# Optimization experiments

Measured on AMD Instinct MI355X. Metric: run time of the kernel, lower is better.

Reference implementation:

```python
import jax, jax.numpy as jnp
import numpy as np

NUM_NODES = 20000
NUM_RELATIONS = 32
HIDDEN = 128
EMB = 16
NUM_EDGES = 600000


def setup_inputs() -> dict:
    key = jax.random.key(0)
    ks = jax.random.split(key, 8)
    edge_index = jax.random.randint(ks[0], (2, NUM_EDGES), 0, NUM_NODES, dtype=jnp.int64)
    edge_type = jax.random.randint(ks[1], (NUM_EDGES,), 0, NUM_RELATIONS, dtype=jnp.int64)
    node_emb = jax.random.normal(ks[2], (NUM_NODES, EMB), dtype=jnp.float32)
    W1 = jax.random.normal(ks[3], (NUM_RELATIONS, EMB, HIDDEN), dtype=jnp.float32) * (1.0 / np.sqrt(EMB))
    root1 = jax.random.normal(ks[4], (EMB, HIDDEN), dtype=jnp.float32) * (1.0 / np.sqrt(EMB))
    b1 = jnp.zeros((HIDDEN,), dtype=jnp.float32)
    W2 = jax.random.normal(ks[5], (NUM_RELATIONS, HIDDEN, HIDDEN), dtype=jnp.float32) * (1.0 / np.sqrt(HIDDEN))
    root2 = jax.random.normal(ks[6], (HIDDEN, HIDDEN), dtype=jnp.float32) * (1.0 / np.sqrt(HIDDEN))
    b2 = jnp.zeros((HIDDEN,), dtype=jnp.float32)
    return {"edge_index": edge_index, "edge_type": edge_type, "node_emb": node_emb,
            "W1": W1, "root1": root1, "b1": b1, "W2": W2, "root2": root2, "b2": b2}


def rgcn_layer(x, edge_index, edge_type, W, root, bias):
    # PyG RGCNConv: per-relation transform, per-(dst, relation) MEAN aggregation,
    # summed over relations, plus root transform and bias.
    src, dst = edge_index[0], edge_index[1]
    # mean normalization per (dst, relation) segment
    seg = dst * NUM_RELATIONS + edge_type                      # [E]
    counts = jax.ops.segment_sum(jnp.ones(seg.shape, jnp.float32), seg,
                                 num_segments=NUM_NODES * NUM_RELATIONS)
    inv = jnp.where(counts > 0, 1.0 / counts, 0.0)
    # transform every node by every relation weight: [N, R, H]
    xr = jnp.einsum('nf,rfh->nrh', x, W)
    msg = xr[src, edge_type] * inv[seg][:, None]               # [E, H]
    agg = jax.ops.segment_sum(msg, dst, num_segments=NUM_NODES)  # [N, H]
    return agg + x @ root + bias


def reference(edge_index, edge_type, node_emb, W1, root1, b1, W2, root2, b2):
    h = rgcn_layer(node_emb, edge_index, edge_type, W1, root1, b1)
    h = jax.nn.relu(h)
    h = rgcn_layer(h, edge_index, edge_type, W2, root2, b2)
    return h
```

## Files before the change

### kernel.cpp

```cpp
#include <hip/hip_runtime.h>
#include <hip/hip_bf16.h>

#define N_NODES 20000
#define N_REL 32
#define HID 128
#define EMB 16
#define N_EDGES 600000
#define NB (N_NODES * N_REL)

typedef __attribute__((ext_vector_type(8))) short  bf8v;
typedef __attribute__((ext_vector_type(8))) unsigned short us8v;
typedef __attribute__((ext_vector_type(4))) unsigned short us4v;
typedef __attribute__((ext_vector_type(4))) float  f4v;

__device__ __forceinline__ unsigned short f2b(float f) {
    __hip_bfloat16 h = __float2bfloat16(f);
    return __builtin_bit_cast(unsigned short, h);
}
__device__ __forceinline__ float b2f(unsigned short u) {
    unsigned int x = ((unsigned int)u) << 16;
    return __builtin_bit_cast(float, x);
}

__device__ __forceinline__ void lds_barrier() {
    asm volatile("s_waitcnt lgkmcnt(0)\n\ts_barrier" ::: "memory");
}

#define R_W2 (N_REL * HID * HID)
#define R_XB (N_NODES * 32)
#define R_W1 (N_REL * HID * 32)
#define R_R1 (HID * 32)
#define R_R2 (HID * HID)
#define R_HIST N_EDGES
#define PRE_TOT (R_W2 + R_XB + R_W1 + R_R1 + R_R2 + R_HIST)

__global__ __launch_bounds__(256) void pre1_k(
    const int* __restrict__ dst, const int* __restrict__ et,
    const float* __restrict__ x, const float* __restrict__ W1,
    const float* __restrict__ root1, const float* __restrict__ W2,
    const float* __restrict__ root2,
    int* __restrict__ hist,
    unsigned short* __restrict__ xb, unsigned short* __restrict__ w1t,
    unsigned short* __restrict__ r1t, unsigned short* __restrict__ w2t,
    unsigned short* __restrict__ r2t) {
    int i = blockIdx.x * 256 + threadIdx.x;
    if (i < R_W2) {
        int r = i >> 14, k = (i >> 7) & 127, n = i & 127;
        int ct8 = n >> 4, m16 = n & 15, ks = k >> 5, q = (k >> 3) & 3, j = k & 7;
        w2t[(size_t)r * 16384 + (ct8 * 4 + ks) * 512 + m16 * 32 + q * 8 + j] = f2b(W2[i]);
        return;
    }
    i -= R_W2;
    if (i < R_XB) {
        int n = i >> 5, k = i & 31;
        xb[i] = (k < EMB) ? f2b(x[n * EMB + k]) : (unsigned short)0;
        return;
    }
    i -= R_XB;
    if (i < R_W1) {
        int r = i >> 12, rem = i & 4095;
        int ct8 = rem >> 9, m16 = (rem >> 5) & 15, q = (rem >> 3) & 3, j = rem & 7;
        int n = ct8 * 16 + m16, k = q * 8 + j;
        w1t[i] = (k < EMB) ? f2b(W1[(r << 11) + (k << 7) + n]) : (unsigned short)0;
        return;
    }
    i -= R_W1;
    if (i < R_R1) {
        int ct8 = i >> 9, m16 = (i >> 5) & 15, q = (i >> 3) & 3, j = i & 7;
        int n = ct8 * 16 + m16, k = q * 8 + j;
        r1t[i] = (k < EMB) ? f2b(root1[(k << 7) + n]) : (unsigned short)0;
        return;
    }
    i -= R_R1;
    if (i < R_R2) {
        int ct8 = i >> 11, ks = (i >> 9) & 3, m16 = (i >> 5) & 15, q = (i >> 3) & 3, j = i & 7;
        int n = ct8 * 16 + m16, k = ks * 32 + q * 8 + j;
        r2t[i] = f2b(root2[(k << 7) + n]);
        return;
    }
    i -= R_R2;
    if (i < R_HIST) atomicAdd(&hist[dst[i] * N_REL + et[i]], 1);
}

__global__ void scan1_k(const int* __restrict__ hist, int* __restrict__ binoff,
                        int* __restrict__ bsum, float* __restrict__ inv) {
    __shared__ int sh[256];
    const int t = threadIdx.x;
    const int base = blockIdx.x * 1024 + t * 4;
    int4 h4 = *(const int4*)(hist + base);
    float4 iv4;
    iv4.x = h4.x > 0 ? 1.0f / h4.x : 0.0f;
    iv4.y = h4.y > 0 ? 1.0f / h4.y : 0.0f;
    iv4.z = h4.z > 0 ? 1.0f / h4.z : 0.0f;
    iv4.w = h4.w > 0 ? 1.0f / h4.w : 0.0f;
    *(float4*)(inv + base) = iv4;
    int ts = h4.x + h4.y + h4.z + h4.w;
    sh[t] = ts;
    __syncthreads();
    for (int o = 1; o < 256; o <<= 1) {
        int v = (t >= o) ? sh[t - o] : 0;
        __syncthreads();
        sh[t] += v;
        __syncthreads();
    }
    int exc = sh[t] - ts;
    binoff[base + 0] = exc;
    binoff[base + 1] = exc + h4.x;
    binoff[base + 2] = exc + h4.x + h4.y;
    binoff[base + 3] = exc + h4.x + h4.y + h4.z;
    if (t == 255) bsum[blockIdx.x] = sh[255];
}

__global__ void scan2_k(const int* __restrict__ bsum, int* __restrict__ bbase) {
    __shared__ int sh[1024];
    const int t = threadIdx.x;
    int v = (t < 625) ? bsum[t] : 0;
    sh[t] = v;
    __syncthreads();
    for (int o = 1; o < 1024; o <<= 1) {
        int u = (t >= o) ? sh[t - o] : 0;
        __syncthreads();
        sh[t] += u;
        __syncthreads();
    }
    if (t < 625) bbase[t] = sh[t] - v;
}

__global__ void scan3_k(int* __restrict__ binoff, const int* __restrict__ bbase,
                        int* __restrict__ cursors) {
    int i = blockIdx.x * 256 + threadIdx.x;
    if (i < NB) {
        int v = binoff[i] + bbase[i >> 10];
        binoff[i] = v;
        cursors[i] = v;
    }
    if (i == 0) binoff[NB] = N_EDGES;
}

__global__ void scatter_k(const int* __restrict__ src, const int* __restrict__ dst,
                          const int* __restrict__ et, int* __restrict__ cursors,
                          int* __restrict__ ssrc) {
    int e = blockIdx.x * 256 + threadIdx.x;
    if (e < 4) ssrc[N_EDGES + e] = 0;
    if (e < N_EDGES) {
        int b = dst[e] * N_REL + et[e];
        int p = atomicAdd(&cursors[b], 1);
        ssrc[p] = src[e];
    }
}

template<int KT, int LSS, int CW, int RG>
__global__ __launch_bounds__(256) void gemm_f(
    const int* __restrict__ binoff, const float* __restrict__ inv,
    const int* __restrict__ ssrc,
    const unsigned short* __restrict__ G,
    const unsigned short* __restrict__ Bw,
    const unsigned short* __restrict__ Br,
    float* __restrict__ part) {

    constexpr int ROW = KT * 32;
    constexpr int NCH = ROW / CW;
    constexpr int CP8 = CW / 8;
    static_assert(NCH * CW == ROW, "chunk covering must be exact");
    static_assert(32 * NCH <= 256, "one gather item per thread");

    __shared__ __align__(16) unsigned short As[2][32 * LSS];
    __shared__ int   smO[32 * (RG + 1)];
    __shared__ float smI[32 * RG];

    const int t = threadIdx.x;
    const int w = t >> 6, lane = t & 63;
    const int q = lane >> 4, m16 = lane & 15;
    const int d0 = blockIdx.x * 32;
    const int r0 = blockIdx.y * RG;
    const bool isLast = (blockIdx.y == gridDim.y - 1);
    const int colb = w * 32;
    const int cb16 = colb >> 4;
    const int fo = m16 * 32 + q * 8;
    const bool gat = t < 32 * NCH;
    const int grow = t / NCH, gcc = t % NCH;
    const int mb  = grow * (RG + 1);
    const int mbI = grow * RG;
    int uo[CP8];
#pragma unroll
    for (int j = 0; j < CP8; ++j) uo[j] = (gcc + j * NCH) * 8;

    for (int i = t; i < 32 * (RG + 1); i += 256) {
        int row = i / (RG + 1), rr = i % (RG + 1);
        smO[i] = binoff[(d0 + row) * N_REL + r0 + rr];
    }
    for (int i = t; i < 32 * RG; i += 256) {
        int row = i / RG, rr = i % RG;
        smI[i] = inv[(d0 + row) * N_REL + r0 + rr];
    }
    lds_barrier();

    f4v acc[2][2];
#pragma unroll
    for (int rt = 0; rt < 2; ++rt)
#pragma unroll
        for (int ct = 0; ct < 2; ++ct) acc[rt][ct] = f4v{0.f, 0.f, 0.f, 0.f};

    us8v gE[4][CP8];
#pragma unroll
    for (int e = 0; e < 4; ++e)
#pragma unroll
        for (int j = 0; j < CP8; ++j) gE[e][j] = us8v{};
    int sx[4] = {0, 0, 0, 0};

    if (gat) {
        const int so = smO[mb], cnt = smO[mb + 1] - so;
        int s0 = ssrc[so], s1 = ssrc[so + 1], s2 = ssrc[so + 2], s3 = ssrc[so + 3];
        if (cnt >= 1) {
            const unsigned short* gp = G + (size_t)s0 * ROW;
#pragma unroll
            for (int j = 0; j < CP8; ++j) gE[0][j] = *(const us8v*)(gp + uo[j]);
        }
        if (cnt >= 2) {
            const unsigned short* gp = G + (size_t)s1 * ROW;
#pragma unroll
            for (int j = 0; j < CP8; ++j) gE[1][j] = *(const us8v*)(gp + uo[j]);
        }
        if (cnt >= 3) {
            const unsigned short* gp = G + (size_t)s2 * ROW;
#pragma unroll
            for (int j = 0; j < CP8; ++j) gE[2][j] = *(const us8v*)(gp + uo[j]);
        }
        if (cnt >= 4) {
            const unsigned short* gp = G + (size_t)s3 * ROW;
#pragma unroll
            for (int j = 0; j < CP8; ++j) gE[3][j] = *(const us8v*)(gp + uo[j]);
        }
        if (RG > 1) {
            const int so1 = smO[mb + 1];
            sx[0] = ssrc[so1]; sx[1] = ssrc[so1 + 1];
            sx[2] = ssrc[so1 + 2]; sx[3] = ssrc[so1 + 3];
        }
    }

    bf8v bfr[2][KT];
#pragma unroll
    for (int ct = 0; ct < 2; ++ct) {
#pragma unroll
        for (int ks = 0; ks < KT; ++ks)
            bfr[ct][ks] = *(const bf8v*)(Bw + (size_t)r0 * (HID * ROW)
                              + ((cb16 + ct) * KT + ks) * 512 + fo);
    }

    for (int it = 0; it < RG; ++it) {
        unsigned short* Ab = As[it & 1];
        if (gat) {
            const int so = smO[mb + it], eo = smO[mb + it + 1];
            const int cnt = eo - so;
            const float m2 = cnt >= 2 ? 1.f : 0.f;
            const float m3 = cnt >= 3 ? 1.f : 0.f;
            const float m4 = cnt >= 4 ? 1.f : 0.f;
            float a[CW];
#pragma unroll
            for (int j = 0; j < CP8; ++j)
#pragma unroll
                for (int k = 0; k < 8; ++k)
                    a[j * 8 + k] = b2f(gE[0][j][k]) + m2 * b2f(gE[1][j][k])
                                 + m3 * b2f(gE[2][j][k]) + m4 * b2f(gE[3][j][k]);
            for (int p = so + 4; p < eo; ++p) {
                const unsigned short* gp = G + (size_t)ssrc[p] * ROW;
#pragma unroll
                for (int j = 0; j < CP8; ++j) {
                    us8v g = *(const us8v*)(gp + uo[j]);
#pragma unroll
                    for (int k = 0; k < 8; ++k) a[j * 8 + k] += b2f(g[k]);
                }
            }
            const float iv = smI[mbI + it];
            unsigned short* wp = &Ab[grow * LSS];
#pragma unroll
            for (int j = 0; j < CP8; ++j) {
                us8v sv;
#pragma unroll
                for (int k = 0; k < 8; ++k) sv[k] = f2b(a[j * 8 + k] * iv);
                *(us8v*)(wp + uo[j]) = sv;
            }

            if (it + 1 < RG) {
                const int c1 = smO[mb + it + 2] - smO[mb + it + 1];
                if (c1 >= 1) {
                    const unsigned short* gp = G + (size_t)sx[0] * ROW;
#pragma unroll
                    for (int j = 0; j < CP8; ++j) gE[0][j] = *(const us8v*)(gp + uo[j]);
                }
                if (c1 >= 2) {
                    const unsigned short* gp = G + (size_t)sx[1] * ROW;
#pragma unroll
                    for (int j = 0; j < CP8; ++j) gE[1][j] = *(const us8v*)(gp + uo[j]);
                }
                if (c1 >= 3) {
                    const unsigned short* gp = G + (size_t)sx[2] * ROW;
#pragma unroll
                    for (int j = 0; j < CP8; ++j) gE[2][j] = *(const us8v*)(gp + uo[j]);
                }
                if (c1 >= 4) {
                    const unsigned short* gp = G + (size_t)sx[3] * ROW;
#pragma unroll
                    for (int j = 0; j < CP8; ++j) gE[3][j] = *(const us8v*)(gp + uo[j]);
                }
                if (it + 2 < RG) {
                    const int so2 = smO[mb + it + 2];
                    sx[0] = ssrc[so2]; sx[1] = ssrc[so2 + 1];
                    sx[2] = ssrc[so2 + 2]; sx[3] = ssrc[so2 + 3];
                }
            }
        }
        lds_barrier();

#pragma unroll
        for (int rt = 0; rt < 2; ++rt) {
            const unsigned short* ar = &Ab[(m16 + 16 * rt) * LSS];
#pragma unroll
            for (int ks = 0; ks < KT; ++ks) {
                bf8v af = *(const bf8v*)(ar + ks * 32 + q * 8);
                acc[rt][0] = __builtin_amdgcn_mfma_f32_16x16x32_bf16(af, bfr[0][ks], acc[rt][0], 0, 0, 0);
                acc[rt][1] = __builtin_amdgcn_mfma_f32_16x16x32_bf16(af, bfr[1][ks], acc[rt][1], 0, 0, 0);
            }
        }

        const unsigned short* Bp = (it + 1 < RG) ? (Bw + (size_t)(r0 + it + 1) * (HID * ROW))
                                                 : (isLast ? Br : nullptr);
        if (Bp) {
#pragma unroll
            for (int ct = 0; ct < 2; ++ct) {
#pragma unroll
                for (int ks = 0; ks < KT; ++ks)
                    bfr[ct][ks] = *(const bf8v*)(Bp + ((cb16 + ct) * KT + ks) * 512 + fo);
            }
        }
    }

    if (isLast) {
#pragma unroll
        for (int rt = 0; rt < 2; ++rt) {
#pragma unroll
            for (int ks = 0; ks < KT; ++ks) {
                bf8v af = *(const bf8v*)(G + (size_t)(d0 + m16 + 16 * rt) * ROW + ks * 32 + q * 8);
                acc[rt][0] = __builtin_amdgcn_mfma_f32_16x16x32_bf16(af, bfr[0][ks], acc[rt][0], 0, 0, 0);
                acc[rt][1] = __builtin_amdgcn_mfma_f32_16x16x32_bf16(af, bfr[1][ks], acc[rt][1], 0, 0, 0);
            }
        }
    }

    float* pb = part + (size_t)blockIdx.y * N_NODES * HID;
#pragma unroll
    for (int ct = 0; ct < 2; ++ct) {
        const int col = colb + 16 * ct + m16;
#pragma unroll
        for (int rt = 0; rt < 2; ++rt) {
#pragma unroll
            for (int g = 0; g < 4; ++g) {
                const int rr = 16 * rt + q * 4 + g;
                __builtin_nontemporal_store(acc[rt][ct][g],
                    &pb[(size_t)(d0 + rr) * HID + col]);
            }
        }
    }
}

__global__ __launch_bounds__(256) void reduce1_k(
    const float* __restrict__ part, const float* __restrict__ b1,
    unsigned short* __restrict__ h1b) {
    int i = blockIdx.x * 256 + threadIdx.x;
    if (i >= N_NODES * HID / 4) return;
    const size_t S = (size_t)N_NODES * HID;
    float4 bb = *(const float4*)(b1 + ((i * 4) & 127));
    float r0 = bb.x, r1 = bb.y, r2 = bb.z, r3 = bb.w;
#pragma unroll
    for (int p = 0; p < 2; ++p) {
        const float* pp = part + p * S + (size_t)i * 4;
        r0 += __builtin_nontemporal_load(pp + 0);
        r1 += __builtin_nontemporal_load(pp + 1);
        r2 += __builtin_nontemporal_load(pp + 2);
        r3 += __builtin_nontemporal_load(pp + 3);
    }
    us4v v;
    v[0] = f2b(fmaxf(r0, 0.0f));
    v[1] = f2b(fmaxf(r1, 0.0f));
    v[2] = f2b(fmaxf(r2, 0.0f));
    v[3] = f2b(fmaxf(r3, 0.0f));
    *(us4v*)(h1b + (size_t)i * 4) = v;
}

__global__ __launch_bounds__(256) void reduce2_k(
    const float* __restrict__ part, const float* __restrict__ b2,
    float* __restrict__ out) {
    int i = blockIdx.x * 256 + threadIdx.x;
    if (i >= N_NODES * HID / 4) return;
    const size_t S = (size_t)N_NODES * HID;
    float4 bb = *(const float4*)(b2 + ((i * 4) & 127));
    float r0 = bb.x, r1 = bb.y, r2 = bb.z, r3 = bb.w;
#pragma unroll
    for (int p = 0; p < 4; ++p) {
        const float* pp = part + p * S + (size_t)i * 4;
        r0 += __builtin_nontemporal_load(pp + 0);
        r1 += __builtin_nontemporal_load(pp + 1);
        r2 += __builtin_nontemporal_load(pp + 2);
        r3 += __builtin_nontemporal_load(pp + 3);
    }
    float4 r; r.x = r0; r.y = r1; r.z = r2; r.w = r3;
    ((float4*)out)[i] = r;
}

extern "C" void kernel_launch(void* const* d_in, const int* in_sizes, int n_in,
                              void* d_out, int out_size, void* d_ws, size_t ws_size,
                              hipStream_t stream) {
    const int*   ei    = (const int*)d_in[0];
    const int*   et    = (const int*)d_in[1];
    const float* x     = (const float*)d_in[2];
    const float* W1    = (const float*)d_in[3];
    const float* root1 = (const float*)d_in[4];
    const float* b1    = (const float*)d_in[5];
    const float* W2    = (const float*)d_in[6];
    const float* root2 = (const float*)d_in[7];
    const float* b2    = (const float*)d_in[8];
    float* out = (float*)d_out;

    char* ws = (char*)d_ws;
    size_t off = 0;
    auto alloc = [&](size_t bytes) { void* p = ws + off; off = (off + bytes + 63) & ~(size_t)63; return p; };
    int*   hist    = (int*)  alloc((size_t)NB * 4);
    int*   binoff  = (int*)  alloc((size_t)(NB + 1) * 4);
    int*   cursors = (int*)  alloc((size_t)NB * 4);
    float* inv     = (float*)alloc((size_t)NB * 4);
    int*   bsum    = (int*)  alloc(625 * 4);
    int*   bbase   = (int*)  alloc(625 * 4);
    int*   ssrc    = (int*)  alloc((size_t)(N_EDGES + 4) * 4);
    unsigned short* xb  = (unsigned short*)alloc((size_t)N_NODES * 32 * 2);
    unsigned short* h1b = (unsigned short*)alloc((size_t)N_NODES * HID * 2);
    unsigned short* w1t = (unsigned short*)alloc((size_t)N_REL * HID * 32 * 2);
    unsigned short* r1t = (unsigned short*)alloc((size_t)HID * 32 * 2);
    unsigned short* w2t = (unsigned short*)alloc((size_t)N_REL * HID * HID * 2);
    unsigned short* r2t = (unsigned short*)alloc((size_t)HID * HID * 2);
    float* part = (float*)alloc((size_t)4 * N_NODES * HID * 4);

    const int* src = ei;
    const int* dst = ei + N_EDGES;

    hipMemsetAsync(hist, 0, (size_t)NB * 4, stream);
    pre1_k<<<(PRE_TOT + 255) / 256, 256, 0, stream>>>(
        dst, et, x, W1, root1, W2, root2, hist, xb, w1t, r1t, w2t, r2t);
    scan1_k<<<NB / 1024, 256, 0, stream>>>(hist, binoff, bsum, inv);
    scan2_k<<<1, 1024, 0, stream>>>(bsum, bbase);
    scan3_k<<<(NB + 255) / 256, 256, 0, stream>>>(binoff, bbase, cursors);
    scatter_k<<<(N_EDGES + 255) / 256, 256, 0, stream>>>(src, dst, et, cursors, ssrc);

    gemm_f<1, 40, 8, 16><<<dim3(625, 2), 256, 0, stream>>>(
        binoff, inv, ssrc, xb, w1t, r1t, part);
    reduce1_k<<<(N_NODES * HID / 4 + 255) / 256, 256, 0, stream>>>(part, b1, h1b);

    gemm_f<4, 136, 16, 8><<<dim3(625, 4), 256, 0, stream>>>(
        binoff, inv, ssrc, h1b, w2t, r2t, part);
    reduce2_k<<<(N_NODES * HID / 4 + 255) / 256, 256, 0, stream>>>(part, b2, out);
}
```

Before: 247.0 us.

## Pack multiple relations per K-tile in layer 1 and fuse its reduction

Layer 1 used to zero-pad the 16-wide embedding to 32 so that each MFMA K-step carried one relation. It now packs two relations, each 16 wide, into every K=32 step and gathers 8 relation segments per iteration in unpadded bf16. Layer 1 runs as a single grid column, so bias, ReLU and the bf16 cast are applied in the epilogue, which removes the partial buffer and the reduce1 kernel. The weight layouts are rebuilt to a K-block-major order to match, and root1 is zero-padded for the partial K tile. The aim is to halve the wasted MFMA and gather work in layer 1 and cut one launch plus its memory traffic, at the cost of less grid parallelism for layer 1.

```diff
diff --git a/kernel.cpp b/kernel.cpp
--- a/kernel.cpp
+++ b/kernel.cpp
@@ -27,8 +27,8 @@
 }
 
 #define R_W2 (N_REL * HID * HID)
-#define R_XB (N_NODES * 32)
-#define R_W1 (N_REL * HID * 32)
+#define R_XB (N_NODES * EMB)
+#define R_W1 (N_REL * EMB * HID)
 #define R_R1 (HID * 32)
 #define R_R2 (HID * HID)
 #define R_HIST N_EDGES
@@ -46,36 +46,34 @@
     int i = blockIdx.x * 256 + threadIdx.x;
     if (i < R_W2) {
         int r = i >> 14, k = (i >> 7) & 127, n = i & 127;
-        int ct8 = n >> 4, m16 = n & 15, ks = k >> 5, q = (k >> 3) & 3, j = k & 7;
-        w2t[(size_t)r * 16384 + (ct8 * 4 + ks) * 512 + m16 * 32 + q * 8 + j] = f2b(W2[i]);
+        int kb = r * 4 + (k >> 5), q = (k >> 3) & 3, j = k & 7;
+        int ct8 = n >> 4, m16 = n & 15;
+        w2t[(size_t)kb * 4096 + ct8 * 512 + m16 * 32 + q * 8 + j] = f2b(W2[i]);
         return;
     }
     i -= R_W2;
-    if (i < R_XB) {
-        int n = i >> 5, k = i & 31;
-        xb[i] = (k < EMB) ? f2b(x[n * EMB + k]) : (unsigned short)0;
-        return;
-    }
+    if (i < R_XB) { xb[i] = f2b(x[i]); return; }
     i -= R_XB;
     if (i < R_W1) {
-        int r = i >> 12, rem = i & 4095;
-        int ct8 = rem >> 9, m16 = (rem >> 5) & 15, q = (rem >> 3) & 3, j = rem & 7;
-        int n = ct8 * 16 + m16, k = q * 8 + j;
-        w1t[i] = (k < EMB) ? f2b(W1[(r << 11) + (k << 7) + n]) : (unsigned short)0;
+        int rel = i >> 11, kk = (i >> 7) & 15, n = i & 127;
+        int kb = rel >> 1, k = ((rel & 1) << 4) + kk;
+        int q = k >> 3, j = k & 7, ct8 = n >> 4, m16 = n & 15;
+        w1t[kb * 4096 + ct8 * 512 + m16 * 32 + q * 8 + j] = f2b(W1[i]);
         return;
     }
     i -= R_W1;
     if (i < R_R1) {
-        int ct8 = i >> 9, m16 = (i >> 5) & 15, q = (i >> 3) & 3, j = i & 7;
-        int n = ct8 * 16 + m16, k = q * 8 + j;
-        r1t[i] = (k < EMB) ? f2b(root1[(k << 7) + n]) : (unsigned short)0;
+        int k = i >> 7, n = i & 127;
+        int q = k >> 3, j = k & 7, ct8 = n >> 4, m16 = n & 15;
+        r1t[ct8 * 512 + m16 * 32 + q * 8 + j] =
+            (k < EMB) ? f2b(root1[k * 128 + n]) : (unsigned short)0;
         return;
     }
     i -= R_R1;
     if (i < R_R2) {
-        int ct8 = i >> 11, ks = (i >> 9) & 3, m16 = (i >> 5) & 15, q = (i >> 3) & 3, j = i & 7;
-        int n = ct8 * 16 + m16, k = ks * 32 + q * 8 + j;
-        r2t[i] = f2b(root2[(k << 7) + n]);
+        int k = i >> 7, n = i & 127;
+        int ks = k >> 5, q = (k >> 3) & 3, j = k & 7, ct8 = n >> 4, m16 = n & 15;
+        r2t[(ks * 8 + ct8) * 512 + m16 * 32 + q * 8 + j] = f2b(root2[i]);
         return;
     }
     i -= R_R2;
@@ -149,20 +147,26 @@
     }
 }
 
-template<int KT, int LSS, int CW, int RG>
+template<int ROWG, int NRC, int NIT, int KR, bool FUSE>
 __global__ __launch_bounds__(256) void gemm_f(
     const int* __restrict__ binoff, const float* __restrict__ inv,
     const int* __restrict__ ssrc,
     const unsigned short* __restrict__ G,
     const unsigned short* __restrict__ Bw,
     const unsigned short* __restrict__ Br,
-    float* __restrict__ part) {
-
-    constexpr int ROW = KT * 32;
-    constexpr int NCH = ROW / CW;
+    float* __restrict__ part, unsigned short* __restrict__ fout,
+    const float* __restrict__ bias) {
+
+    constexpr int RG  = NRC * NIT;
+    constexpr int KT  = (NRC * ROWG) / 32;
+    constexpr int NCH = 256 / (32 * NRC);
+    constexpr int CW  = ROWG / NCH;
     constexpr int CP8 = CW / 8;
-    static_assert(NCH * CW == ROW, "chunk covering must be exact");
-    static_assert(32 * NCH <= 256, "one gather item per thread");
+    constexpr int LSS = NRC * ROWG + 8;
+    static_assert(NCH * CW == ROWG, "chunk covering must be exact");
+    static_assert(CP8 * 8 == CW, "16B unit covering");
+    static_assert(KT * 32 == NRC * ROWG, "K must be a multiple of 32");
+    static_assert(32 * NRC * NCH == 256, "all threads gather");
 
     __shared__ __align__(16) unsigned short As[2][32 * LSS];
     __shared__ int   smO[32 * (RG + 1)];
@@ -177,13 +181,15 @@
     const int colb = w * 32;
     const int cb16 = colb >> 4;
     const int fo = m16 * 32 + q * 8;
-    const bool gat = t < 32 * NCH;
-    const int grow = t / NCH, gcc = t % NCH;
-    const int mb  = grow * (RG + 1);
-    const int mbI = grow * RG;
+    const int brow = t / (NRC * NCH);
+    const int rsub = (t / NCH) % NRC;
+    const int gcc  = t % NCH;
+    const int mb  = brow * (RG + 1) + rsub;
+    const int mbI = brow * RG + rsub;
     int uo[CP8];
 #pragma unroll
     for (int j = 0; j < CP8; ++j) uo[j] = (gcc + j * NCH) * 8;
+    const int lbase = brow * LSS + rsub * ROWG;
 
     for (int i = t; i < 32 * (RG + 1); i += 256) {
         int row = i / (RG + 1), rr = i % (RG + 1);
@@ -208,49 +214,51 @@
         for (int j = 0; j < CP8; ++j) gE[e][j] = us8v{};
     int sx[4] = {0, 0, 0, 0};
 
-    if (gat) {
+    {
         const int so = smO[mb], cnt = smO[mb + 1] - so;
         int s0 = ssrc[so], s1 = ssrc[so + 1], s2 = ssrc[so + 2], s3 = ssrc[so + 3];
         if (cnt >= 1) {
-            const unsigned short* gp = G + (size_t)s0 * ROW;
+            const unsigned short* gp = G + (size_t)s0 * ROWG;
 #pragma unroll
             for (int j = 0; j < CP8; ++j) gE[0][j] = *(const us8v*)(gp + uo[j]);
         }
         if (cnt >= 2) {
-            const unsigned short* gp = G + (size_t)s1 * ROW;
+            const unsigned short* gp = G + (size_t)s1 * ROWG;
 #pragma unroll
             for (int j = 0; j < CP8; ++j) gE[1][j] = *(const us8v*)(gp + uo[j]);
         }
         if (cnt >= 3) {
-            const unsigned short* gp = G + (size_t)s2 * ROW;
+            const unsigned short* gp = G + (size_t)s2 * ROWG;
 #pragma unroll
             for (int j = 0; j < CP8; ++j) gE[2][j] = *(const us8v*)(gp + uo[j]);
         }
         if (cnt >= 4) {
-            const unsigned short* gp = G + (size_t)s3 * ROW;
+            const unsigned short* gp = G + (size_t)s3 * ROWG;
 #pragma unroll
             for (int j = 0; j < CP8; ++j) gE[3][j] = *(const us8v*)(gp + uo[j]);
         }
-        if (RG > 1) {
-            const int so1 = smO[mb + 1];
+        if (NIT > 1) {
+            const int so1 = smO[mb + NRC];
             sx[0] = ssrc[so1]; sx[1] = ssrc[so1 + 1];
             sx[2] = ssrc[so1 + 2]; sx[3] = ssrc[so1 + 3];
         }
     }
 
     bf8v bfr[2][KT];
-#pragma unroll
-    for (int ct = 0; ct < 2; ++ct) {
-#pragma unroll
-        for (int ks = 0; ks < KT; ++ks)
-            bfr[ct][ks] = *(const bf8v*)(Bw + (size_t)r0 * (HID * ROW)
-                              + ((cb16 + ct) * KT + ks) * 512 + fo);
-    }
-
-    for (int it = 0; it < RG; ++it) {
+    {
+        const int kb0 = (r0 * ROWG) >> 5;
+#pragma unroll
+        for (int ct = 0; ct < 2; ++ct) {
+#pragma unroll
+            for (int ks = 0; ks < KT; ++ks)
+                bfr[ct][ks] = *(const bf8v*)(Bw + ((size_t)(kb0 + ks) * 8 + cb16 + ct) * 512 + fo);
+        }
+    }
+
+    for (int it = 0; it < NIT; ++it) {
         unsigned short* Ab = As[it & 1];
-        if (gat) {
-            const int so = smO[mb + it], eo = smO[mb + it + 1];
+        {
+            const int so = smO[mb + it * NRC], eo = smO[mb + it * NRC + 1];
             const int cnt = eo - so;
             const float m2 = cnt >= 2 ? 1.f : 0.f;
             const float m3 = cnt >= 3 ? 1.f : 0.f;
@@ -263,7 +271,7 @@
                     a[j * 8 + k] = b2f(gE[0][j][k]) + m2 * b2f(gE[1][j][k])
                                  + m3 * b2f(gE[2][j][k]) + m4 * b2f(gE[3][j][k]);
             for (int p = so + 4; p < eo; ++p) {
-                const unsigned short* gp = G + (size_t)ssrc[p] * ROW;
+                const unsigned short* gp = G + (size_t)ssrc[p] * ROWG;
 #pragma unroll
                 for (int j = 0; j < CP8; ++j) {
                     us8v g = *(const us8v*)(gp + uo[j]);
@@ -271,8 +279,8 @@
                     for (int k = 0; k < 8; ++k) a[j * 8 + k] += b2f(g[k]);
                 }
             }
-            const float iv = smI[mbI + it];
-            unsigned short* wp = &Ab[grow * LSS];
+            const float iv = smI[mbI + it * NRC];
+            unsigned short* wp = &Ab[lbase];
 #pragma unroll
             for (int j = 0; j < CP8; ++j) {
                 us8v sv;
@@ -281,30 +289,31 @@
                 *(us8v*)(wp + uo[j]) = sv;
             }
 
-            if (it + 1 < RG) {
-                const int c1 = smO[mb + it + 2] - smO[mb + it + 1];
+            if (it + 1 < NIT) {
+                const int b1o = mb + (it + 1) * NRC;
+                const int c1 = smO[b1o + 1] - smO[b1o];
                 if (c1 >= 1) {
-                    const unsigned short* gp = G + (size_t)sx[0] * ROW;
+                    const unsigned short* gp = G + (size_t)sx[0] * ROWG;
 #pragma unroll
                     for (int j = 0; j < CP8; ++j) gE[0][j] = *(const us8v*)(gp + uo[j]);
                 }
                 if (c1 >= 2) {
-                    const unsigned short* gp = G + (size_t)sx[1] * ROW;
+                    const unsigned short* gp = G + (size_t)sx[1] * ROWG;
 #pragma unroll
                     for (int j = 0; j < CP8; ++j) gE[1][j] = *(const us8v*)(gp + uo[j]);
                 }
                 if (c1 >= 3) {
-                    const unsigned short* gp = G + (size_t)sx[2] * ROW;
+                    const unsigned short* gp = G + (size_t)sx[2] * ROWG;
 #pragma unroll
                     for (int j = 0; j < CP8; ++j) gE[2][j] = *(const us8v*)(gp + uo[j]);
                 }
                 if (c1 >= 4) {
-                    const unsigned short* gp = G + (size_t)sx[3] * ROW;
+                    const unsigned short* gp = G + (size_t)sx[3] * ROWG;
 #pragma unroll
                     for (int j = 0; j < CP8; ++j) gE[3][j] = *(const us8v*)(gp + uo[j]);
                 }
-                if (it + 2 < RG) {
-                    const int so2 = smO[mb + it + 2];
+                if (it + 2 < NIT) {
+                    const int so2 = smO[mb + (it + 2) * NRC];
                     sx[0] = ssrc[so2]; sx[1] = ssrc[so2 + 1];
                     sx[2] = ssrc[so2 + 2]; sx[3] = ssrc[so2 + 3];
                 }
@@ -323,14 +332,20 @@
             }
         }
 
-        const unsigned short* Bp = (it + 1 < RG) ? (Bw + (size_t)(r0 + it + 1) * (HID * ROW))
-                                                 : (isLast ? Br : nullptr);
-        if (Bp) {
+        if (it + 1 < NIT) {
+            const int kb0 = ((r0 + (it + 1) * NRC) * ROWG) >> 5;
 #pragma unroll
             for (int ct = 0; ct < 2; ++ct) {
 #pragma unroll
                 for (int ks = 0; ks < KT; ++ks)
-                    bfr[ct][ks] = *(const bf8v*)(Bp + ((cb16 + ct) * KT + ks) * 512 + fo);
+                    bfr[ct][ks] = *(const bf8v*)(Bw + ((size_t)(kb0 + ks) * 8 + cb16 + ct) * 512 + fo);
+            }
+        } else if (isLast) {
+#pragma unroll
+            for (int ct = 0; ct < 2; ++ct) {
+#pragma unroll
+                for (int ks = 0; ks < KR; ++ks)
+                    bfr[ct][ks] = *(const bf8v*)(Br + ((size_t)ks * 8 + cb16 + ct) * 512 + fo);
             }
         }
     }
@@ -338,53 +353,54 @@
     if (isLast) {
 #pragma unroll
         for (int rt = 0; rt < 2; ++rt) {
-#pragma unroll
-            for (int ks = 0; ks < KT; ++ks) {
-                bf8v af = *(const bf8v*)(G + (size_t)(d0 + m16 + 16 * rt) * ROW + ks * 32 + q * 8);
+            const unsigned short* gr = G + (size_t)(d0 + m16 + 16 * rt) * ROWG;
+#pragma unroll
+            for (int ks = 0; ks < KR; ++ks) {
+                bf8v af;
+                if constexpr (ROWG % 32 == 0) {
+                    af = *(const bf8v*)(gr + ks * 32 + q * 8);
+                } else {
+                    af = bf8v{0, 0, 0, 0, 0, 0, 0, 0};
+                    if (ks * 32 + q * 8 + 8 <= ROWG)
+                        af = *(const bf8v*)(gr + ks * 32 + q * 8);
+                }
                 acc[rt][0] = __builtin_amdgcn_mfma_f32_16x16x32_bf16(af, bfr[0][ks], acc[rt][0], 0, 0, 0);
                 acc[rt][1] = __builtin_amdgcn_mfma_f32_16x16x32_bf16(af, bfr[1][ks], acc[rt][1], 0, 0, 0);
             }
         }
     }
 
-    float* pb = part + (size_t)blockIdx.y * N_NODES * HID;
-#pragma unroll
-    for (int ct = 0; ct < 2; ++ct) {
-        const int col = colb + 16 * ct + m16;
-#pragma unroll
-        for (int rt = 0; rt < 2; ++rt) {
-#pragma unroll
-            for (int g = 0; g < 4; ++g) {
-                const int rr = 16 * rt + q * 4 + g;
-                __builtin_nontemporal_store(acc[rt][ct][g],
-                    &pb[(size_t)(d0 + rr) * HID + col]);
-            }
-        }
-    }
-}
-
-__global__ __launch_bounds__(256) void reduce1_k(
-    const float* __restrict__ part, const float* __restrict__ b1,
-    unsigned short* __restrict__ h1b) {
-    int i = blockIdx.x * 256 + threadIdx.x;
-    if (i >= N_NODES * HID / 4) return;
-    const size_t S = (size_t)N_NODES * HID;
-    float4 bb = *(const float4*)(b1 + ((i * 4) & 127));
-    float r0 = bb.x, r1 = bb.y, r2 = bb.z, r3 = bb.w;
-#pragma unroll
-    for (int p = 0; p < 2; ++p) {
-        const float* pp = part + p * S + (size_t)i * 4;
-        r0 += __builtin_nontemporal_load(pp + 0);
-        r1 += __builtin_nontemporal_load(pp + 1);
-        r2 += __builtin_nontemporal_load(pp + 2);
-        r3 += __builtin_nontemporal_load(pp + 3);
-    }
-    us4v v;
-    v[0] = f2b(fmaxf(r0, 0.0f));
-    v[1] = f2b(fmaxf(r1, 0.0f));
-    v[2] = f2b(fmaxf(r2, 0.0f));
-    v[3] = f2b(fmaxf(r3, 0.0f));
-    *(us4v*)(h1b + (size_t)i * 4) = v;
+    if constexpr (FUSE) {
+#pragma unroll
+        for (int ct = 0; ct < 2; ++ct) {
+            const int col = colb + 16 * ct + m16;
+            const float bb = bias[col];
+#pragma unroll
+            for (int rt = 0; rt < 2; ++rt) {
+#pragma unroll
+                for (int g = 0; g < 4; ++g) {
+                    const int rr = 16 * rt + q * 4 + g;
+                    fout[(size_t)(d0 + rr) * HID + col] =
+                        f2b(fmaxf(acc[rt][ct][g] + bb, 0.0f));
+                }
+            }
+        }
+    } else {
+        float* pb = part + (size_t)blockIdx.y * N_NODES * HID;
+#pragma unroll
+        for (int ct = 0; ct < 2; ++ct) {
+            const int col = colb + 16 * ct + m16;
+#pragma unroll
+            for (int rt = 0; rt < 2; ++rt) {
+#pragma unroll
+                for (int g = 0; g < 4; ++g) {
+                    const int rr = 16 * rt + q * 4 + g;
+                    __builtin_nontemporal_store(acc[rt][ct][g],
+                        &pb[(size_t)(d0 + rr) * HID + col]);
+                }
+            }
+        }
+    }
 }
 
 __global__ __launch_bounds__(256) void reduce2_k(
@@ -431,9 +447,9 @@
     int*   bsum    = (int*)  alloc(625 * 4);
     int*   bbase   = (int*)  alloc(625 * 4);
     int*   ssrc    = (int*)  alloc((size_t)(N_EDGES + 4) * 4);
-    unsigned short* xb  = (unsigned short*)alloc((size_t)N_NODES * 32 * 2);
+    unsigned short* xb  = (unsigned short*)alloc((size_t)N_NODES * EMB * 2);
     unsigned short* h1b = (unsigned short*)alloc((size_t)N_NODES * HID * 2);
-    unsigned short* w1t = (unsigned short*)alloc((size_t)N_REL * HID * 32 * 2);
+    unsigned short* w1t = (unsigned short*)alloc((size_t)R_W1 * 2);
     unsigned short* r1t = (unsigned short*)alloc((size_t)HID * 32 * 2);
     unsigned short* w2t = (unsigned short*)alloc((size_t)N_REL * HID * HID * 2);
     unsigned short* r2t = (unsigned short*)alloc((size_t)HID * HID * 2);
@@ -450,11 +466,10 @@
     scan3_k<<<(NB + 255) / 256, 256, 0, stream>>>(binoff, bbase, cursors);
     scatter_k<<<(N_EDGES + 255) / 256, 256, 0, stream>>>(src, dst, et, cursors, ssrc);
 
-    gemm_f<1, 40, 8, 16><<<dim3(625, 2), 256, 0, stream>>>(
-        binoff, inv, ssrc, xb, w1t, r1t, part);
-    reduce1_k<<<(N_NODES * HID / 4 + 255) / 256, 256, 0, stream>>>(part, b1, h1b);
-
-    gemm_f<4, 136, 16, 8><<<dim3(625, 4), 256, 0, stream>>>(
-        binoff, inv, ssrc, h1b, w2t, r2t, part);
+    gemm_f<16, 8, 4, 1, true><<<dim3(625, 1), 256, 0, stream>>>(
+        binoff, inv, ssrc, xb, w1t, r1t, nullptr, h1b, b1);
+
+    gemm_f<128, 1, 8, 4, false><<<dim3(625, 4), 256, 0, stream>>>(
+        binoff, inv, ssrc, h1b, w2t, r2t, part, nullptr, nullptr);
     reduce2_k<<<(N_NODES * HID / 4 + 255) / 256, 256, 0, stream>>>(part, b2, out);
 }
```

New measurement: 243.8 us. About the same (-1.3%).
